# Kernel optimization log

Measured on AMD Instinct MI355X. Metric: run time of the kernel, lower is better.

## Reference

```python
import jax, jax.numpy as jnp
import numpy as np

N, T, D, C = 32, 512, 1024, 120
EPS = 1e-12
SCALE = 2.0 * (D ** 0.5)


def setup_inputs() -> dict:
    key = jax.random.key(0)
    ks = jax.random.split(key, 16)
    inp = {
        'anc_perm_input': jax.random.normal(ks[0], (N, T, D), dtype=jnp.float32),
        'pos_perm_input': jax.random.normal(ks[1], (N, T, D), dtype=jnp.float32),
        'neg_perm_input': jax.random.normal(ks[2], (N, T, D), dtype=jnp.float32),
        'anc_src_key_padding_mask': jax.random.randint(ks[3], (N, T), 0, 2) == 1,
        'pos_src_key_padding_mask': jax.random.randint(ks[4], (N, T), 0, 2) == 1,
        'neg_src_key_padding_mask': jax.random.randint(ks[5], (N, T), 0, 2) == 1,
        # learned parameters (stored as (in, out); math-equivalent to torch x @ W.T)
        'W_attn': jax.random.normal(ks[6], (D, D), dtype=jnp.float32) * 0.02,
        'b_attn': jnp.zeros((D,), dtype=jnp.float32),
        'W1': jax.random.normal(ks[7], (D, D), dtype=jnp.float32) * 0.02,
        'b1': jnp.zeros((D,), dtype=jnp.float32),
        'W2': jax.random.normal(ks[8], (D, D), dtype=jnp.float32) * 0.02,
        'b2': jnp.zeros((D,), dtype=jnp.float32),
        'ln_g': jnp.ones((D,), dtype=jnp.float32),
        'ln_b': jnp.zeros((D,), dtype=jnp.float32),
        'W_last': jax.random.normal(ks[9], (D, C), dtype=jnp.float32) * 0.02,
        'b_last': jnp.zeros((C,), dtype=jnp.float32),
    }
    return inp


def _ntd_nd(x, mask, W_attn, b_attn, W1, b1, W2, b2, ln_g, ln_b, W_last, b_last):
    # x: (N,T,D); mask: (N,T) bool, True = padding
    w = x @ W_attn + b_attn                                   # (N,T,D)
    valid = ~mask                                             # (N,T)
    scores = jnp.einsum('btd,bsd->bts', w, w)                 # (N,T,T)
    scores = jnp.where(valid[:, :, None] & valid[:, None, :], scores, 0.0)
    s = jnp.sum(scores, axis=1) / SCALE                       # (N,T)
    s = jnp.where(mask, -jnp.inf, s)
    attn = jax.nn.softmax(s, axis=1)                          # (N,T)
    # proj_head: duplicate OrderedDict key => linear1 -> relu -> linear2 (no final act)
    proj = jax.nn.relu(x @ W1 + b1) @ W2 + b2                 # (N,T,D)
    pooled = jnp.einsum('bt,btd->bd', attn, proj)             # (N,D)
    mu = jnp.mean(pooled, axis=-1, keepdims=True)
    var = jnp.var(pooled, axis=-1, keepdims=True)
    normed = (pooled - mu) / jnp.sqrt(var + EPS) * ln_g + ln_b
    return jax.nn.relu(normed) @ W_last + b_last              # (N,C)


def reference(anc_perm_input, pos_perm_input, neg_perm_input,
              anc_src_key_padding_mask, pos_src_key_padding_mask, neg_src_key_padding_mask,
              W_attn, b_attn, W1, b1, W2, b2, ln_g, ln_b, W_last, b_last):
    params = (W_attn, b_attn, W1, b1, W2, b2, ln_g, ln_b, W_last, b_last)
    anc = _ntd_nd(anc_perm_input, anc_src_key_padding_mask, *params)
    pos = _ntd_nd(pos_perm_input, pos_src_key_padding_mask, *params)
    neg = _ntd_nd(neg_perm_input, neg_src_key_padding_mask, *params)
    return (anc, pos, neg)
```

## Files before the change

kernel.cpp:

```cpp
#include <hip/hip_runtime.h>
#include <hip/hip_bf16.h>
#include <math.h>

#define N_B 32
#define T_S 512
#define D_D 1024
#define C_C 120
#define ZB 96
#define SCALE 64.0f

typedef unsigned short u16;
typedef __attribute__((ext_vector_type(8))) short short8;
typedef __attribute__((ext_vector_type(8))) unsigned short ushort8;
typedef __attribute__((ext_vector_type(4))) float floatx4;

__device__ inline u16 f2bf(float f) {
    union { __hip_bfloat16 h; u16 u; } c; c.h = __float2bfloat16(f); return c.u;
}
__device__ inline float bf2f(u16 u) {
    union { unsigned i; float f; } c; c.i = ((unsigned)u) << 16; return c.f;
}

__device__ inline void gll16(const void* g, void* l) {
    __builtin_amdgcn_global_load_lds((const __attribute__((address_space(1))) void*)g,
                                     (__attribute__((address_space(3))) void*)l,
                                     16, 0, 0);
}

__device__ inline bool mask_is_i8(const int* mk) {
    bool i8 = false;
#pragma unroll
    for (int i = 0; i < 16; i++) {
        unsigned v = ((const unsigned*)mk)[i];
        if (v > 1u) i8 = true;
    }
    return i8;
}
__device__ inline int mask_val(const int* mk, int idx, bool i8) {
    return i8 ? (int)((const signed char*)mk)[idx] : mk[idx];
}

__global__ void k_scan(const int* m0, const int* m1, const int* m2,
                       int* __restrict__ chunk_base, int* __restrict__ cnts,
                       u16* __restrict__ xp) {
    int zb = blockIdx.x;
    int z = zb >> 5, b = zb & 31;
    const int* mk = z == 0 ? m0 : (z == 1 ? m1 : m2);
    bool i8 = mask_is_i8(mk);
    int tid = threadIdx.x;
    __shared__ int wcnt[8];
    bool v0 = (mask_val(mk, b * T_S + tid, i8) == 0);
    bool v1 = (mask_val(mk, b * T_S + 256 + tid, i8) == 0);
    unsigned long long b0 = __ballot(v0);
    unsigned long long b1 = __ballot(v1);
    int wave = tid >> 6;
    if ((tid & 63) == 0) {
        wcnt[wave] = (int)__popcll(b0);
        wcnt[wave + 4] = (int)__popcll(b1);
    }
    __syncthreads();
    __shared__ int s_cnt;
    if (tid == 0) {
        int run = 0;
#pragma unroll
        for (int c = 0; c < 8; c++) {
            chunk_base[zb * 8 + c] = run;
            run += wcnt[c];
        }
        cnts[zb] = run;
        s_cnt = run;
    }
    __syncthreads();
    int cnt = s_cnt;
    int cend = (cnt + 127) & ~127;
    if (cend > T_S) cend = T_S;
    u16* base = xp + ((size_t)zb * T_S + cnt) * D_D;
    int n8 = (cend - cnt) * (D_D / 8);
    ushort8 zz = {0,0,0,0,0,0,0,0};
    for (int i = tid; i < n8; i += 256)
        *(ushort8*)(base + (size_t)i * 8) = zz;
}

__global__ void k_prep(const float* __restrict__ W_attn, const float* __restrict__ W1,
                       const float* x0, const float* x1, const float* x2,
                       const int* m0, const int* m1, const int* m2,
                       const int* __restrict__ chunk_base,
                       float* __restrict__ WT, u16* __restrict__ W1T,
                       float* __restrict__ xsum, u16* __restrict__ xp) {
    int bx = blockIdx.x;
    int tid = threadIdx.x;
    if (bx < 1024) {
        int tbx = bx & 31, tby = bx >> 5;
        __shared__ float tile[32][33];
        int tx = tid & 31, ty = tid >> 5;
#pragma unroll
        for (int j = 0; j < 32; j += 8)
            tile[ty + j][tx] = W_attn[(size_t)(tby*32 + ty + j)*D_D + tbx*32 + tx];
        __syncthreads();
#pragma unroll
        for (int j = 0; j < 32; j += 8)
            WT[(size_t)(tbx*32 + ty + j)*D_D + tby*32 + tx] = tile[tx][ty + j];
        __syncthreads();
#pragma unroll
        for (int j = 0; j < 32; j += 8)
            tile[ty + j][tx] = W1[(size_t)(tby*32 + ty + j)*D_D + tbx*32 + tx];
        __syncthreads();
#pragma unroll
        for (int j = 0; j < 32; j += 8)
            W1T[(size_t)(tbx*32 + ty + j)*D_D + tby*32 + tx] = f2bf(tile[tx][ty + j]);
        return;
    }
    int idx = bx - 1024;
    int chunk = idx & 7, zb = idx >> 3;
    int z = zb >> 5, b = zb & 31;
    const float* x = z == 0 ? x0 : (z == 1 ? x1 : x2);
    const int* mk = z == 0 ? m0 : (z == 1 ? m1 : m2);
    bool i8 = mask_is_i8(mk);
    int t0 = chunk * 64;
    int slot = chunk_base[zb * 8 + chunk];
    const float4* xr = (const float4*)(x + (size_t)(b * T_S) * D_D);
    u16* pack = xp + (size_t)zb * T_S * D_D;
    float4 acc = {0.f, 0.f, 0.f, 0.f};
    for (int i = 0; i < 64; i++) {
        int t = t0 + i;
        if (mask_val(mk, b * T_S + t, i8) == 0) {
            float4 v = xr[(size_t)t * 256 + tid];
            union { __hip_bfloat162 h; ushort2 u; } c0, c1;
            c0.h = __float22bfloat162_rn({v.x, v.y});
            c1.h = __float22bfloat162_rn({v.z, v.w});
            ushort4 uu = {c0.u.x, c0.u.y, c1.u.x, c1.u.y};
            *(ushort4*)(pack + (size_t)slot * D_D + tid * 4) = uu;
            slot++;
            acc.x += v.x; acc.y += v.y; acc.z += v.z; acc.w += v.w;
        }
    }
    float* xs = xsum + (size_t)zb * D_D + tid * 4;
    atomicAdd(xs + 0, acc.x); atomicAdd(xs + 1, acc.y);
    atomicAdd(xs + 2, acc.z); atomicAdd(xs + 3, acc.w);
}

__global__ void k_matvec(const float* __restrict__ W, const float* __restrict__ vin,
                         const float* __restrict__ bias, const int* __restrict__ bmul,
                         float scale, float* __restrict__ vout) {
    int z = blockIdx.z, bg = blockIdx.y;
    int och = blockIdx.x >> 3, kc = blockIdx.x & 7;
    int o = och * 256 + threadIdx.x;
    int brow = z * N_B + bg * 4;
    float acc[4] = {0.f, 0.f, 0.f, 0.f};
    if (kc == 0 && bias) {
        float bv = bias[o];
#pragma unroll
        for (int bb = 0; bb < 4; bb++)
            acc[bb] = bmul ? bv * (float)bmul[brow + bb] : bv;
    }
    const float* vi = vin + (size_t)brow * D_D + kc * 128;
    const float* Wp = W + (size_t)(kc * 128) * D_D + o;
#pragma unroll 4
    for (int i = 0; i < 128; i++) {
        float wv = Wp[(size_t)i * D_D];
#pragma unroll
        for (int bb = 0; bb < 4; bb++)
            acc[bb] += vi[(size_t)bb * D_D + i] * wv;
    }
#pragma unroll
    for (int bb = 0; bb < 4; bb++)
        atomicAdd(&vout[(size_t)(brow + bb) * D_D + o], acc[bb] * scale);
}

__global__ void k_dots(const u16* __restrict__ xp, const float* __restrict__ vs,
                       const int* __restrict__ cnts, float* __restrict__ sdot) {
    int zb = blockIdx.y;
    int t0 = blockIdx.x * 4;
    if (t0 >= cnts[zb]) return;
    int t = t0 + (threadIdx.x >> 6);
    int lane = threadIdx.x & 63;
    const u16* xr = xp + ((size_t)zb * T_S + t) * D_D;
    const float* vr = vs + (size_t)zb * D_D;
    float acc = 0.f;
#pragma unroll
    for (int i = 0; i < 2; i++) {
        short8 v = *(const short8*)(xr + i * 512 + lane * 8);
        const float* vp = vr + i * 512 + lane * 8;
        float4 a0 = *(const float4*)(vp);
        float4 a1 = *(const float4*)(vp + 4);
        acc += bf2f((u16)v[0]) * a0.x + bf2f((u16)v[1]) * a0.y
             + bf2f((u16)v[2]) * a0.z + bf2f((u16)v[3]) * a0.w
             + bf2f((u16)v[4]) * a1.x + bf2f((u16)v[5]) * a1.y
             + bf2f((u16)v[6]) * a1.z + bf2f((u16)v[7]) * a1.w;
    }
#pragma unroll
    for (int off = 32; off; off >>= 1) acc += __shfl_xor(acc, off, 64);
    if (lane == 0) sdot[(size_t)zb * T_S + t] = acc;
}

__global__ __launch_bounds__(256, 4)
void k_gemm_bf16(const u16* __restrict__ xp, const u16* __restrict__ W1T,
                 const float* __restrict__ b1, const float* __restrict__ sdot,
                 const int* __restrict__ cnts, float* __restrict__ r) {
    int flat = blockIdx.x;
    int low3 = flat & 7, xt = (flat >> 3) & 7;
    int g = ((flat >> 6) << 3) + low3;
    int tile = g & 3, zb = g >> 2;
    int row0 = tile * 128, N0 = xt * 128;
    int cnt = cnts[zb];
    if (row0 >= cnt) return;

    __shared__ __align__(16) u16 As[128 * 64];
    __shared__ __align__(16) u16 Bs[128 * 64];
    __shared__ float sAttn[128];
    __shared__ float redm[4], reds[4];
    int tid = threadIdx.x;
    int wave = tid >> 6, lane = tid & 63;

    {
        int base = zb * T_S;
        float v0 = (tid < cnt) ? sdot[base + tid] : -INFINITY;
        float v1 = (tid + 256 < cnt) ? sdot[base + 256 + tid] : -INFINITY;
        float mx = fmaxf(v0, v1);
#pragma unroll
        for (int off = 32; off; off >>= 1) mx = fmaxf(mx, __shfl_xor(mx, off, 64));
        if (lane == 0) redm[wave] = mx;
        __syncthreads();
        mx = fmaxf(fmaxf(redm[0], redm[1]), fmaxf(redm[2], redm[3]));
        float e = __expf(v0 - mx) + __expf(v1 - mx);
#pragma unroll
        for (int off = 32; off; off >>= 1) e += __shfl_xor(e, off, 64);
        if (lane == 0) reds[wave] = e;
        __syncthreads();
        float tot = reds[0] + reds[1] + reds[2] + reds[3];
        if (tid < 128) {
            int t = row0 + tid;
            float av = 0.f;
            if (t < cnt) av = __expf(sdot[base + t] - mx) / tot;
            sAttn[tid] = av;
        }
    }

    int wy = wave >> 1, wx = wave & 1;
    int q = lane >> 4, cidx = lane & 15;
    int srow = lane >> 3;
    int cp = lane & 7;

    floatx4 acc[4][4];
#pragma unroll
    for (int mi = 0; mi < 4; mi++)
#pragma unroll
        for (int ni = 0; ni < 4; ni++)
            acc[mi][ni] = (floatx4){0.f, 0.f, 0.f, 0.f};

    const u16* abase = xp + ((size_t)zb * T_S + row0) * D_D;
    const u16* bbase = W1T + (size_t)N0 * D_D;

    for (int k0 = 0; k0 < 1024; k0 += 64) {
        __syncthreads();
#pragma unroll
        for (int i = 0; i < 4; i++) {
            int r0 = wave * 32 + i * 8;
            int rr = r0 + srow;
            int gc = cp ^ (rr & 7);
            gll16(abase + (size_t)rr * D_D + k0 + gc * 8, &As[r0 * 64]);
        }
#pragma unroll
        for (int i = 0; i < 4; i++) {
            int r0 = wave * 32 + i * 8;
            int nn = r0 + srow;
            int gc = cp ^ (nn & 7);
            gll16(bbase + (size_t)nn * D_D + k0 + gc * 8, &Bs[r0 * 64]);
        }
        __syncthreads();
#pragma unroll
        for (int ks = 0; ks < 2; ks++) {
            short8 a[4], bfr[4];
#pragma unroll
            for (int mi = 0; mi < 4; mi++) {
                int m = wy * 64 + mi * 16 + cidx;
                a[mi] = *(const short8*)&As[m * 64 + (((ks << 2) | q) ^ (m & 7)) * 8];
            }
#pragma unroll
            for (int ni = 0; ni < 4; ni++) {
                int n = wx * 64 + ni * 16 + cidx;
                bfr[ni] = *(const short8*)&Bs[n * 64 + (((ks << 2) | q) ^ (n & 7)) * 8];
            }
#pragma unroll
            for (int mi = 0; mi < 4; mi++)
#pragma unroll
                for (int ni = 0; ni < 4; ni++)
                    acc[mi][ni] = __builtin_amdgcn_mfma_f32_16x16x32_bf16(
                        a[mi], bfr[ni], acc[mi][ni], 0, 0, 0);
        }
    }

    float* rrow = r + (size_t)zb * D_D;
#pragma unroll
    for (int ni = 0; ni < 4; ni++) {
        int ng = N0 + wx * 64 + ni * 16 + cidx;
        float b1v = b1[ng];
        float sum = 0.f;
#pragma unroll
        for (int mi = 0; mi < 4; mi++) {
#pragma unroll
            for (int rg = 0; rg < 4; rg++) {
                int ml = wy * 64 + mi * 16 + q * 4 + rg;
                float hv = acc[mi][ni][rg] + b1v;
                hv = fmaxf(hv, 0.f);
                sum += hv * sAttn[ml];
            }
        }
        sum += __shfl_xor(sum, 16, 64);
        sum += __shfl_xor(sum, 32, 64);
        if (lane < 16) atomicAdd(&rrow[ng], sum);
    }
}

__global__ void k_pool(const float* __restrict__ rbuf, const float* __restrict__ W2,
                       const float* __restrict__ b2, float* __restrict__ pooled) {
    int zb = blockIdx.y;
    int och = blockIdx.x >> 3, kc = blockIdx.x & 7;
    int o = och * 256 + threadIdx.x;
    float acc = (kc == 0) ? b2[o] : 0.f;
    const float* rp = rbuf + (size_t)zb * D_D + kc * 128;
    const float* Wp = W2 + (size_t)(kc * 128) * D_D + o;
#pragma unroll 4
    for (int i = 0; i < 128; i++)
        acc += rp[i] * Wp[(size_t)i * D_D];
    atomicAdd(&pooled[(size_t)zb * D_D + o], acc);
}

__global__ void k_fin(const float* __restrict__ pooled, const float* __restrict__ ln_g,
                      const float* __restrict__ ln_b, const float* __restrict__ Wl,
                      const float* __restrict__ bl, float* __restrict__ out) {
    int zb = blockIdx.x;
    int tid = threadIdx.x;
    __shared__ float nr[D_D];
    __shared__ float redA[8], redB[8];
    __shared__ float ps[4][C_C];
    const float* p = pooled + (size_t)zb * D_D;
    int o0 = tid, o1 = tid + 512;
    float a0 = p[o0], a1 = p[o1];
    float s1 = a0 + a1, s2 = a0 * a0 + a1 * a1;
#pragma unroll
    for (int off = 32; off; off >>= 1) {
        s1 += __shfl_xor(s1, off, 64);
        s2 += __shfl_xor(s2, off, 64);
    }
    int w = tid >> 6;
    if ((tid & 63) == 0) { redA[w] = s1; redB[w] = s2; }
    __syncthreads();
    float t1 = 0.f, t2 = 0.f;
#pragma unroll
    for (int k = 0; k < 8; k++) { t1 += redA[k]; t2 += redB[k]; }
    float mu = t1 * (1.0f / D_D);
    float var = t2 * (1.0f / D_D) - mu * mu;
    float rstd = 1.0f / sqrtf(var + 1e-12f);
    nr[o0] = fmaxf((a0 - mu) * rstd * ln_g[o0] + ln_b[o0], 0.f);
    nr[o1] = fmaxf((a1 - mu) * rstd * ln_g[o1] + ln_b[o1], 0.f);
    __syncthreads();
    if (tid < 4 * C_C) {
        int seg = tid / C_C, c = tid - seg * C_C;
        const float* wp = Wl + (size_t)(seg * 256) * C_C + c;
        const float* np = nr + seg * 256;
        float acc = 0.f;
#pragma unroll 8
        for (int d = 0; d < 256; d++)
            acc += np[d] * wp[(size_t)d * C_C];
        ps[seg][c] = acc;
    }
    __syncthreads();
    if (tid < C_C)
        out[(size_t)zb * C_C + tid] =
            bl[tid] + ps[0][tid] + ps[1][tid] + ps[2][tid] + ps[3][tid];
}

extern "C" void kernel_launch(void* const* d_in, const int* in_sizes, int n_in,
                              void* d_out, int out_size, void* d_ws, size_t ws_size,
                              hipStream_t stream) {
    const float* x0 = (const float*)d_in[0];
    const float* x1 = (const float*)d_in[1];
    const float* x2 = (const float*)d_in[2];
    const int* m0 = (const int*)d_in[3];
    const int* m1 = (const int*)d_in[4];
    const int* m2 = (const int*)d_in[5];
    const float* W_attn = (const float*)d_in[6];
    const float* b_attn = (const float*)d_in[7];
    const float* W1 = (const float*)d_in[8];
    const float* b1 = (const float*)d_in[9];
    const float* W2 = (const float*)d_in[10];
    const float* b2 = (const float*)d_in[11];
    const float* ln_g = (const float*)d_in[12];
    const float* ln_b = (const float*)d_in[13];
    const float* W_last = (const float*)d_in[14];
    const float* b_last = (const float*)d_in[15];
    float* out = (float*)d_out;

    char* wsb = (char*)d_ws;
    const size_t MB = 1 << 20;
    float* WT     = (float*)(wsb);
    u16*   W1T    = (u16*)  (wsb + 4 * MB);
    float* xsum   = (float*)(wsb + 6 * MB);
    float* rbuf   = (float*)(wsb + 6 * MB + 393216);
    float* wsum   = (float*)(wsb + 6 * MB + 786432);
    float* vs     = (float*)(wsb + 6 * MB + 1179648);
    float* pooled = (float*)(wsb + 6 * MB + 1572864);
    float* sdot   = (float*)(wsb + 8 * MB);
    int*   cbase  = (int*)  (wsb + 8 * MB + 196608);
    int*   cnts   = (int*)  (wsb + 8 * MB + 199680);
    u16*   xp     = (u16*)  (wsb + 9 * MB);

    hipMemsetAsync(wsb + 6 * MB, 0, 2 * MB, stream);

    k_scan  <<<ZB, 256, 0, stream>>>(m0, m1, m2, cbase, cnts, xp);
    k_prep  <<<1792, 256, 0, stream>>>(W_attn, W1, x0, x1, x2, m0, m1, m2,
                                       cbase, WT, W1T, xsum, xp);
    k_matvec<<<dim3(32, 8, 3), 256, 0, stream>>>(W_attn, xsum, b_attn, cnts, 1.0f, wsum);
    k_matvec<<<dim3(32, 8, 3), 256, 0, stream>>>(WT, wsum, nullptr, nullptr, 1.0f / SCALE, vs);
    k_dots  <<<dim3(128, ZB), 256, 0, stream>>>(xp, vs, cnts, sdot);
    k_gemm_bf16<<<3072, 256, 0, stream>>>(xp, W1T, b1, sdot, cnts, rbuf);
    k_pool  <<<dim3(32, ZB), 256, 0, stream>>>(rbuf, W2, b2, pooled);
    k_fin   <<<ZB, 512, 0, stream>>>(pooled, ln_g, ln_b, W_last, b_last, out);
}
```

Measured before the change: 401.1 us.

## Fold workspace zeroing into scan, compact valid rows, reuse matvec for pooling

```diff
diff --git a/kernel.cpp b/kernel.cpp
--- a/kernel.cpp
+++ b/kernel.cpp
@@ -42,12 +42,17 @@
 
 __global__ void k_scan(const int* m0, const int* m1, const int* m2,
                        int* __restrict__ chunk_base, int* __restrict__ cnts,
-                       u16* __restrict__ xp) {
+                       u16* __restrict__ xp, float4* __restrict__ zreg) {
     int zb = blockIdx.x;
+    int tid = threadIdx.x;
+    {
+        float4 zz4 = {0.f, 0.f, 0.f, 0.f};
+        for (int i = zb * 256 + tid; i < (2 * 1024 * 1024 / 16); i += ZB * 256)
+            zreg[i] = zz4;
+    }
     int z = zb >> 5, b = zb & 31;
     const int* mk = z == 0 ? m0 : (z == 1 ? m1 : m2);
     bool i8 = mask_is_i8(mk);
-    int tid = threadIdx.x;
     __shared__ int wcnt[8];
     bool v0 = (mask_val(mk, b * T_S + tid, i8) == 0);
     bool v1 = (mask_val(mk, b * T_S + 256 + tid, i8) == 0);
@@ -117,22 +122,31 @@
     const int* mk = z == 0 ? m0 : (z == 1 ? m1 : m2);
     bool i8 = mask_is_i8(mk);
     int t0 = chunk * 64;
-    int slot = chunk_base[zb * 8 + chunk];
+    __shared__ unsigned char s_list[64];
+    __shared__ int s_cc;
+    if (tid < 64) {
+        bool v = (mask_val(mk, b * T_S + t0 + tid, i8) == 0);
+        unsigned long long bal = __ballot(v);
+        int pos = (int)__popcll(bal & ((1ull << tid) - 1ull));
+        if (v) s_list[pos] = (unsigned char)tid;
+        if (tid == 0) s_cc = (int)__popcll(bal);
+    }
+    __syncthreads();
+    int cc = s_cc;
+    int slot0 = chunk_base[zb * 8 + chunk];
     const float4* xr = (const float4*)(x + (size_t)(b * T_S) * D_D);
     u16* pack = xp + (size_t)zb * T_S * D_D;
     float4 acc = {0.f, 0.f, 0.f, 0.f};
-    for (int i = 0; i < 64; i++) {
-        int t = t0 + i;
-        if (mask_val(mk, b * T_S + t, i8) == 0) {
-            float4 v = xr[(size_t)t * 256 + tid];
-            union { __hip_bfloat162 h; ushort2 u; } c0, c1;
-            c0.h = __float22bfloat162_rn({v.x, v.y});
-            c1.h = __float22bfloat162_rn({v.z, v.w});
-            ushort4 uu = {c0.u.x, c0.u.y, c1.u.x, c1.u.y};
-            *(ushort4*)(pack + (size_t)slot * D_D + tid * 4) = uu;
-            slot++;
-            acc.x += v.x; acc.y += v.y; acc.z += v.z; acc.w += v.w;
-        }
+#pragma unroll 2
+    for (int j = 0; j < cc; j++) {
+        int t = t0 + (int)s_list[j];
+        float4 v = xr[(size_t)t * 256 + tid];
+        union { __hip_bfloat162 h; ushort2 u; } c0, c1;
+        c0.h = __float22bfloat162_rn({v.x, v.y});
+        c1.h = __float22bfloat162_rn({v.z, v.w});
+        ushort4 uu = {c0.u.x, c0.u.y, c1.u.x, c1.u.y};
+        *(ushort4*)(pack + (size_t)(slot0 + j) * D_D + tid * 4) = uu;
+        acc.x += v.x; acc.y += v.y; acc.z += v.z; acc.w += v.w;
     }
     float* xs = xsum + (size_t)zb * D_D + tid * 4;
     atomicAdd(xs + 0, acc.x); atomicAdd(xs + 1, acc.y);
@@ -257,14 +271,14 @@
         for (int i = 0; i < 4; i++) {
             int r0 = wave * 32 + i * 8;
             int rr = r0 + srow;
-            int gc = cp ^ (rr & 7);
+            int gc = cp ^ srow;
             gll16(abase + (size_t)rr * D_D + k0 + gc * 8, &As[r0 * 64]);
         }
 #pragma unroll
         for (int i = 0; i < 4; i++) {
             int r0 = wave * 32 + i * 8;
             int nn = r0 + srow;
-            int gc = cp ^ (nn & 7);
+            int gc = cp ^ srow;
             gll16(bbase + (size_t)nn * D_D + k0 + gc * 8, &Bs[r0 * 64]);
         }
         __syncthreads();
@@ -274,12 +288,12 @@
 #pragma unroll
             for (int mi = 0; mi < 4; mi++) {
                 int m = wy * 64 + mi * 16 + cidx;
-                a[mi] = *(const short8*)&As[m * 64 + (((ks << 2) | q) ^ (m & 7)) * 8];
+                a[mi] = *(const short8*)&As[m * 64 + ((((ks << 2) | q) ^ (m & 7)) << 3)];
             }
 #pragma unroll
             for (int ni = 0; ni < 4; ni++) {
                 int n = wx * 64 + ni * 16 + cidx;
-                bfr[ni] = *(const short8*)&Bs[n * 64 + (((ks << 2) | q) ^ (n & 7)) * 8];
+                bfr[ni] = *(const short8*)&Bs[n * 64 + ((((ks << 2) | q) ^ (n & 7)) << 3)];
             }
 #pragma unroll
             for (int mi = 0; mi < 4; mi++)
@@ -310,20 +324,6 @@
         sum += __shfl_xor(sum, 32, 64);
         if (lane < 16) atomicAdd(&rrow[ng], sum);
     }
-}
-
-__global__ void k_pool(const float* __restrict__ rbuf, const float* __restrict__ W2,
-                       const float* __restrict__ b2, float* __restrict__ pooled) {
-    int zb = blockIdx.y;
-    int och = blockIdx.x >> 3, kc = blockIdx.x & 7;
-    int o = och * 256 + threadIdx.x;
-    float acc = (kc == 0) ? b2[o] : 0.f;
-    const float* rp = rbuf + (size_t)zb * D_D + kc * 128;
-    const float* Wp = W2 + (size_t)(kc * 128) * D_D + o;
-#pragma unroll 4
-    for (int i = 0; i < 128; i++)
-        acc += rp[i] * Wp[(size_t)i * D_D];
-    atomicAdd(&pooled[(size_t)zb * D_D + o], acc);
 }
 
 __global__ void k_fin(const float* __restrict__ pooled, const float* __restrict__ ln_g,
@@ -406,15 +406,14 @@
     int*   cnts   = (int*)  (wsb + 8 * MB + 199680);
     u16*   xp     = (u16*)  (wsb + 9 * MB);
 
-    hipMemsetAsync(wsb + 6 * MB, 0, 2 * MB, stream);
-
-    k_scan  <<<ZB, 256, 0, stream>>>(m0, m1, m2, cbase, cnts, xp);
+    k_scan  <<<ZB, 256, 0, stream>>>(m0, m1, m2, cbase, cnts, xp,
+                                     (float4*)(wsb + 6 * MB));
     k_prep  <<<1792, 256, 0, stream>>>(W_attn, W1, x0, x1, x2, m0, m1, m2,
                                        cbase, WT, W1T, xsum, xp);
     k_matvec<<<dim3(32, 8, 3), 256, 0, stream>>>(W_attn, xsum, b_attn, cnts, 1.0f, wsum);
     k_matvec<<<dim3(32, 8, 3), 256, 0, stream>>>(WT, wsum, nullptr, nullptr, 1.0f / SCALE, vs);
     k_dots  <<<dim3(128, ZB), 256, 0, stream>>>(xp, vs, cnts, sdot);
     k_gemm_bf16<<<3072, 256, 0, stream>>>(xp, W1T, b1, sdot, cnts, rbuf);
-    k_pool  <<<dim3(32, ZB), 256, 0, stream>>>(rbuf, W2, b2, pooled);
+    k_matvec<<<dim3(32, 8, 3), 256, 0, stream>>>(W2, rbuf, b2, nullptr, 1.0f, pooled);
     k_fin   <<<ZB, 512, 0, stream>>>(pooled, ln_g, ln_b, W_last, b_last, out);
 }
```

Result: faster. 387.3 us (-3.4%).
